# Optimization experiments

Measured on AMD Instinct MI355X. Metric: run time of the kernel, lower is better.

Reference implementation:

```python
import jax, jax.numpy as jnp
import numpy as np
import math

H = 8
D_MODEL = 512
D_K = D_MODEL // H          # 64, per-head value dim
D_QK = D_K // 2             # 32, per-head query/key dim
B, S = 2, 4096


def setup_inputs() -> dict:
    key = jax.random.key(0)
    ks = jax.random.split(key, 20)
    std = 0.02
    inp = {
        'query': jax.random.normal(ks[0], (B, S, D_MODEL), jnp.float32),
        'key':   jax.random.normal(ks[1], (B, S, D_MODEL), jnp.float32),
        'value': jax.random.normal(ks[2], (B, S, D_MODEL), jnp.float32),
        # MLP_q: d_model -> 2*d_model -> d_model/2
        'Wq1': jax.random.normal(ks[3], (D_MODEL, 2 * D_MODEL), jnp.float32) * std,
        'bq1': jnp.zeros((2 * D_MODEL,), jnp.float32),
        'Wq2': jax.random.normal(ks[4], (2 * D_MODEL, D_MODEL // 2), jnp.float32) * std,
        'bq2': jnp.zeros((D_MODEL // 2,), jnp.float32),
        # MLP_k: d_model -> 2*d_model -> d_model/2
        'Wk1': jax.random.normal(ks[5], (D_MODEL, 2 * D_MODEL), jnp.float32) * std,
        'bk1': jnp.zeros((2 * D_MODEL,), jnp.float32),
        'Wk2': jax.random.normal(ks[6], (2 * D_MODEL, D_MODEL // 2), jnp.float32) * std,
        'bk2': jnp.zeros((D_MODEL // 2,), jnp.float32),
        # linear_v and output linear: d_model -> d_model
        'Wv': jax.random.normal(ks[7], (D_MODEL, D_MODEL), jnp.float32) * std,
        'bv': jnp.zeros((D_MODEL,), jnp.float32),
        'Wo': jax.random.normal(ks[8], (D_MODEL, D_MODEL), jnp.float32) * std,
        'bo': jnp.zeros((D_MODEL,), jnp.float32),
    }
    return inp


def reference(query, key, value, Wq1, bq1, Wq2, bq2, Wk1, bk1, Wk2, bk2, Wv, bv, Wo, bo):
    nb = query.shape[0]
    # MLP_q / MLP_k: Linear -> exact GELU -> Linear (torch GELU default is erf)
    q = jax.nn.gelu(query @ Wq1 + bq1, approximate=False) @ Wq2 + bq2   # [B,S,D_MODEL/2]
    k = jax.nn.gelu(key   @ Wk1 + bk1, approximate=False) @ Wk2 + bk2   # [B,S,D_MODEL/2]
    v = value @ Wv + bv                                                  # [B,S,D_MODEL]

    q = q.reshape(nb, -1, H, D_QK)   # [B,S,H,d_qk]
    k = k.reshape(nb, -1, H, D_QK)
    v = v.reshape(nb, -1, H, D_K)    # [B,S,H,d_k]

    # scores scaled by sqrt(d_qk) since query.size(-1) == d_k//2 in the original
    scores = jnp.einsum('bqhd,bkhd->bhqk', q, k) / math.sqrt(D_QK)  # [B,H,S,S]
    p = jax.nn.softmax(scores, axis=-1)
    x = jnp.einsum('bhqk,bkhd->bqhd', p, v).reshape(nb, -1, H * D_K)  # [B,S,D_MODEL]
    return x @ Wo + bo
```

## Files before the change

### kernel.cpp

```cpp
#include <hip/hip_runtime.h>
#include <math.h>

typedef __attribute__((ext_vector_type(8))) short short8;
typedef __bf16 bf16x8 __attribute__((ext_vector_type(8)));
typedef __attribute__((ext_vector_type(4))) float f32x4;
typedef __attribute__((ext_vector_type(2))) float f32x2;
typedef __attribute__((ext_vector_type(16))) float f32x16;
typedef __attribute__((ext_vector_type(4))) unsigned uint4v;

__device__ inline short f2bf(float f) {
    unsigned u = __builtin_bit_cast(unsigned, f);
    u += 0x7fff + ((u >> 16) & 1);
    return (short)(u >> 16);
}
__device__ inline float bf2f(short h) {
    return __builtin_bit_cast(float, ((unsigned)(unsigned short)h) << 16);
}
__device__ inline float gelu_f(float x) {
    return 0.5f * x * (1.f + erff(x * 0.70710678118654752f));
}

__device__ inline void gload_lds16(const void* g, void* l) {
    __builtin_amdgcn_global_load_lds(
        (const __attribute__((address_space(1))) unsigned int*)g,
        (__attribute__((address_space(3))) unsigned int*)l, 16, 0, 0);
}

__global__ __launch_bounds__(256) void prep_all(
    const float* __restrict__ q, const float* __restrict__ k,
    const float* __restrict__ v,
    short* __restrict__ qc, short* __restrict__ kc, short* __restrict__ vc,
    const float* __restrict__ Wq1, const float* __restrict__ Wk1,
    const float* __restrict__ Wq2, const float* __restrict__ Wk2,
    const float* __restrict__ Wv,  const float* __restrict__ Wo,
    short* __restrict__ Wq1t, short* __restrict__ Wk1t,
    short* __restrict__ Wq2t, short* __restrict__ Wk2t,
    short* __restrict__ Wvt,  short* __restrict__ Wot)
{
    int id = blockIdx.x;
    if (id < 6144) {
        const float* src = id < 2048 ? q : (id < 4096 ? k : v);
        short* dst = id < 2048 ? qc : (id < 4096 ? kc : vc);
        int blk = id & 2047;
        size_t i = ((size_t)blk * 256 + threadIdx.x) * 8;
        float4 a = *(const float4*)(src + i);
        float4 b = *(const float4*)(src + i + 4);
        short8 o;
        o[0] = f2bf(a.x); o[1] = f2bf(a.y); o[2] = f2bf(a.z); o[3] = f2bf(a.w);
        o[4] = f2bf(b.x); o[5] = f2bf(b.y); o[6] = f2bf(b.z); o[7] = f2bf(b.w);
        *(short8*)(void*)(dst + i) = o;
        return;
    }
    id -= 6144;
    const float* W; short* Wt; int K, N;
    if (id < 512)       { W = Wq1; Wt = Wq1t; K = 512;  N = 1024; }
    else if (id < 1024) { W = Wk1; Wt = Wk1t; K = 512;  N = 1024; id -= 512; }
    else if (id < 1280) { W = Wq2; Wt = Wq2t; K = 1024; N = 256;  id -= 1024; }
    else if (id < 1536) { W = Wk2; Wt = Wk2t; K = 1024; N = 256;  id -= 1280; }
    else if (id < 1792) { W = Wv;  Wt = Wvt;  K = 512;  N = 512;  id -= 1536; }
    else                { W = Wo;  Wt = Wot;  K = 512;  N = 512;  id -= 1792; }
    int nx = N >> 5;
    int n0 = (id % nx) * 32, k0 = (id / nx) * 32;

    __shared__ float T[32][33];
    int tid = threadIdx.x;
    int r = tid >> 3, c4 = (tid & 7) * 4;
    float4 v4 = *(const float4*)&W[(size_t)(k0 + r) * N + n0 + c4];
    T[r][c4 + 0] = v4.x; T[r][c4 + 1] = v4.y; T[r][c4 + 2] = v4.z; T[r][c4 + 3] = v4.w;
    __syncthreads();
    short4 o;
    o.x = f2bf(T[c4 + 0][r]);
    o.y = f2bf(T[c4 + 1][r]);
    o.z = f2bf(T[c4 + 2][r]);
    o.w = f2bf(T[c4 + 3][r]);
    *(short4*)&Wt[(size_t)(n0 + r) * K + k0 + c4] = o;
}

template <int ACT, int OUTF32, int BM, int BN>
__global__ __launch_bounds__(256) void gemm_bt(
    const short* __restrict__ A0, const short* __restrict__ A1,
    const short* __restrict__ B0, const short* __restrict__ B1,
    const float* __restrict__ b0, const float* __restrict__ b1,
    void* C0_, void* C1_,
    float s0, float s1, int nbn, int N, int K)
{
    constexpr int MT = BM / 32;
    constexpr int NT = BN / 32;
    const int z = blockIdx.z;
    const short* A = z ? A1 : A0;
    const short* B = z ? B1 : B0;
    const float* bias = z ? b1 : b0;
    void* C_ = z ? C1_ : C0_;
    const float scale = z ? s1 : s0;

    const int L = blockIdx.x;
    const int xcd = L & 7;
    const int per = L >> 3;
    const int bn = (per % nbn) * BN;
    const int bm = ((per / nbn) * 8 + xcd) * BM;

    const int tid = threadIdx.x;
    const int w = tid >> 6;
    const int lane = tid & 63;
    const int l15 = lane & 15, quad = lane >> 4;
    const int wm = (w >> 1) * (BM / 2), wn = (w & 1) * (BN / 2);

    __shared__ __align__(16) short As[BM * 64];
    __shared__ __align__(16) short Bs[BN * 64];

    f32x4 acc[MT][NT];
#pragma unroll
    for (int mt = 0; mt < MT; ++mt)
#pragma unroll
        for (int nt = 0; nt < NT; ++nt) acc[mt][nt] = (f32x4){0.f, 0.f, 0.f, 0.f};

    for (int k0 = 0; k0 < K; k0 += 64) {
#pragma unroll
        for (int i = 0; i < BM / 32; ++i) {
            int ga = tid + i * 256;
            int row = ga >> 3, g = ga & 7;
            gload_lds16(&A[(size_t)(bm + row) * K + k0 + ((g ^ (row & 7)) * 8)],
                        &As[(i * 256 + w * 64) * 8]);
        }
#pragma unroll
        for (int i = 0; i < BN / 32; ++i) {
            int gb = tid + i * 256;
            int row = gb >> 3, g = gb & 7;
            gload_lds16(&B[(size_t)(bn + row) * K + k0 + ((g ^ (row & 7)) * 8)],
                        &Bs[(i * 256 + w * 64) * 8]);
        }
        __syncthreads();

#pragma unroll
        for (int ks = 0; ks < 2; ++ks) {
            bf16x8 af[MT], bfr[NT];
#pragma unroll
            for (int t = 0; t < MT; ++t) {
                int row = wm + t * 16 + l15;
                af[t] = __builtin_bit_cast(bf16x8,
                    *(const short8*)(const void*)&As[row * 64 + (((ks * 4 + quad) ^ (row & 7)) * 8)]);
            }
#pragma unroll
            for (int t = 0; t < NT; ++t) {
                int row = wn + t * 16 + l15;
                bfr[t] = __builtin_bit_cast(bf16x8,
                    *(const short8*)(const void*)&Bs[row * 64 + (((ks * 4 + quad) ^ (row & 7)) * 8)]);
            }
#pragma unroll
            for (int mt = 0; mt < MT; ++mt)
#pragma unroll
                for (int nt = 0; nt < NT; ++nt)
                    acc[mt][nt] = __builtin_amdgcn_mfma_f32_16x16x32_bf16(af[mt], bfr[nt], acc[mt][nt], 0, 0, 0);
        }
        __syncthreads();
    }

    float bv[NT];
#pragma unroll
    for (int nt = 0; nt < NT; ++nt) bv[nt] = bias[bn + wn + nt * 16 + l15];
#pragma unroll
    for (int mt = 0; mt < MT; ++mt)
#pragma unroll
        for (int r = 0; r < 4; ++r) {
            int row = bm + wm + mt * 16 + quad * 4 + r;
#pragma unroll
            for (int nt = 0; nt < NT; ++nt) {
                float v = acc[mt][nt][r] + bv[nt];
                if (ACT) v = gelu_f(v);
                v *= scale;
                int col = bn + wn + nt * 16 + l15;
                if (OUTF32) ((float*)C_)[(size_t)row * N + col] = v;
                else        ((short*)C_)[(size_t)row * N + col] = f2bf(v);
            }
        }
}

__global__ __launch_bounds__(256) void repack_kv(
    const short* __restrict__ kb, short* __restrict__ kfr,
    const short* __restrict__ vbb, short* __restrict__ vfr)
{
    const int kt = blockIdx.x;
    const int y = blockIdx.y;
    const int t = threadIdx.x;
    __shared__ short Vt[64][72];

    if (y < 16) {
        const int bh = y;
        const int b = bh >> 3, h = bh & 7;
        const int c = t >> 6, l = t & 63;
        const int nt = c >> 1, ks = c & 1;
        int key = kt * 64 + nt * 32 + (l & 31);
        int k = ks * 16 + (l >> 5) * 8;
        short8 v = *(const short8*)(const void*)&kb[(size_t)(b * 4096 + key) * 256 + h * 32 + k];
        *(short8*)(void*)&kfr[((((size_t)bh * 64 + kt) * 4 + c) * 64 + l) * 8] = v;
        return;
    }
    const int bh = y - 16;
    const int b = bh >> 3, h = bh & 7;
#pragma unroll
    for (int it = 0; it < 2; ++it) {
        int idx = t + it * 256;
        int keyr = idx >> 3, c8 = (idx & 7) * 8;
        *(short8*)(void*)&Vt[keyr][c8] =
            *(const short8*)(const void*)&vbb[(size_t)(b * 4096 + kt * 64 + keyr) * 512 + h * 64 + c8];
    }
    __syncthreads();
#pragma unroll
    for (int it = 0; it < 2; ++it) {
        int chunk = (t >> 6) * 2 + it;
        int l = t & 63;
        int dt = chunk >> 2, ks = chunk & 3;
        short8 o;
#pragma unroll
        for (int j = 0; j < 8; ++j)
            o[j] = Vt[ks * 16 + (l >> 5) * 8 + j][dt * 32 + (l & 31)];
        *(short8*)(void*)&vfr[((((size_t)bh * 64 + kt) * 8 + chunk) * 64 + l) * 8] = o;
    }
}

__global__ __launch_bounds__(256, 4) void flash_ks(
    const short* __restrict__ qb, const short* __restrict__ kfr,
    const short* __restrict__ vfr, short* __restrict__ xbb)
{
    const int L = blockIdx.x;
    const int xcd = L & 7;
    const int idx = L >> 3;
    const int bh = xcd * 2 + (idx & 1);
    const int qt = idx >> 1;
    const int b = bh >> 3, h = bh & 7;
    const int w = threadIdx.x >> 6;
    const int qg = w >> 1;
    const int kh = w & 1;
    const int lane = threadIdx.x & 63;
    const int l31 = lane & 31;
    const int half = lane >> 5;

    __shared__ __align__(16) char smem[17408];

    const short* qrow = qb + (size_t)(b * 4096 + qt * 64 + qg * 32 + l31) * 256 + h * 32 + half * 8;
    bf16x8 qf0 = __builtin_bit_cast(bf16x8, *(const short8*)(const void*)qrow);
    bf16x8 qf1 = __builtin_bit_cast(bf16x8, *(const short8*)(const void*)(qrow + 16));

    f32x16 O0{}, O1{};
    f32x2 lp = (f32x2){0.f, 0.f};

    const short* kbase = kfr + ((size_t)bh * 64) * 4 * 512 + lane * 8;
    const short* vbase = vfr + ((size_t)bh * 64) * 8 * 512 + lane * 8;

#pragma unroll 1
    for (int t = 0; t < 32; ++t) {
        const int kt = kh * 32 + t;
        bf16x8 kc[4], vc[8];
        const short* kp = kbase + (size_t)kt * 4 * 512;
        const short* vp = vbase + (size_t)kt * 8 * 512;
#pragma unroll
        for (int c = 0; c < 4; ++c)
            kc[c] = __builtin_bit_cast(bf16x8, *(const short8*)(const void*)(kp + c * 512));
#pragma unroll
        for (int c = 0; c < 8; ++c)
            vc[c] = __builtin_bit_cast(bf16x8, *(const short8*)(const void*)(vp + c * 512));

        f32x16 zero{};
        f32x16 s0 = __builtin_amdgcn_mfma_f32_32x32x16_bf16(kc[0], qf0, zero, 0, 0, 0);
        s0 = __builtin_amdgcn_mfma_f32_32x32x16_bf16(kc[1], qf1, s0, 0, 0, 0);
        f32x16 s1 = __builtin_amdgcn_mfma_f32_32x32x16_bf16(kc[2], qf0, zero, 0, 0, 0);
        s1 = __builtin_amdgcn_mfma_f32_32x32x16_bf16(kc[3], qf1, s1, 0, 0, 0);

        bf16x8 pf[4];
#pragma unroll
        for (int nt = 0; nt < 2; ++nt) {
            const f32x16& s = nt ? s1 : s0;
            float p0  = __builtin_amdgcn_exp2f(s[0]);
            float p1  = __builtin_amdgcn_exp2f(s[1]);
            float p2  = __builtin_amdgcn_exp2f(s[2]);
            float p3  = __builtin_amdgcn_exp2f(s[3]);
            float p4  = __builtin_amdgcn_exp2f(s[4]);
            float p5  = __builtin_amdgcn_exp2f(s[5]);
            float p6  = __builtin_amdgcn_exp2f(s[6]);
            float p7  = __builtin_amdgcn_exp2f(s[7]);
            float p8  = __builtin_amdgcn_exp2f(s[8]);
            float p9  = __builtin_amdgcn_exp2f(s[9]);
            float p10 = __builtin_amdgcn_exp2f(s[10]);
            float p11 = __builtin_amdgcn_exp2f(s[11]);
            float p12 = __builtin_amdgcn_exp2f(s[12]);
            float p13 = __builtin_amdgcn_exp2f(s[13]);
            float p14 = __builtin_amdgcn_exp2f(s[14]);
            float p15 = __builtin_amdgcn_exp2f(s[15]);

            lp += (f32x2){p0,  p1};
            lp += (f32x2){p2,  p3};
            lp += (f32x2){p4,  p5};
            lp += (f32x2){p6,  p7};
            lp += (f32x2){p8,  p9};
            lp += (f32x2){p10, p11};
            lp += (f32x2){p12, p13};
            lp += (f32x2){p14, p15};

            unsigned D0, D1, D2, D3, D4, D5, D6, D7;
            asm("v_cvt_pk_bf16_f32 %0, %1, %2" : "=v"(D0) : "v"(p0),  "v"(p1));
            asm("v_cvt_pk_bf16_f32 %0, %1, %2" : "=v"(D1) : "v"(p2),  "v"(p3));
            asm("v_cvt_pk_bf16_f32 %0, %1, %2" : "=v"(D2) : "v"(p4),  "v"(p5));
            asm("v_cvt_pk_bf16_f32 %0, %1, %2" : "=v"(D3) : "v"(p6),  "v"(p7));
            asm("v_cvt_pk_bf16_f32 %0, %1, %2" : "=v"(D4) : "v"(p8),  "v"(p9));
            asm("v_cvt_pk_bf16_f32 %0, %1, %2" : "=v"(D5) : "v"(p10), "v"(p11));
            asm("v_cvt_pk_bf16_f32 %0, %1, %2" : "=v"(D6) : "v"(p12), "v"(p13));
            asm("v_cvt_pk_bf16_f32 %0, %1, %2" : "=v"(D7) : "v"(p14), "v"(p15));
            asm("v_permlane32_swap_b32 %0, %1" : "+v"(D0), "+v"(D2));
            asm("v_permlane32_swap_b32 %0, %1" : "+v"(D1), "+v"(D3));
            asm("v_permlane32_swap_b32 %0, %1" : "+v"(D4), "+v"(D6));
            asm("v_permlane32_swap_b32 %0, %1" : "+v"(D5), "+v"(D7));
            uint4v u0; u0[0] = D0; u0[1] = D1; u0[2] = D2; u0[3] = D3;
            uint4v u1; u1[0] = D4; u1[1] = D5; u1[2] = D6; u1[3] = D7;
            pf[2 * nt + 0] = __builtin_bit_cast(bf16x8, u0);
            pf[2 * nt + 1] = __builtin_bit_cast(bf16x8, u1);
        }

#pragma unroll
        for (int ks = 0; ks < 4; ++ks) {
            O0 = __builtin_amdgcn_mfma_f32_32x32x16_bf16(pf[ks], vc[ks], O0, 0, 0, 0);
            O1 = __builtin_amdgcn_mfma_f32_32x32x16_bf16(pf[ks], vc[4 + ks], O1, 0, 0, 0);
        }
    }

    float lsum = lp[0] + lp[1];
    float lother = lsum;
    asm("v_permlane32_swap_b32 %0, %1" : "+v"(lsum), "+v"(lother));
    lsum += lother;

    float* redO = (float*)smem;
    float* redl = (float*)(smem + 16896);
    if (half == 0)
        redl[(qg * 2 + kh) * 32 + l31] = lsum;
    if (kh == 1) {
        float* Bo = redO + qg * 32 * 66;
#pragma unroll
        for (int r = 0; r < 16; ++r) {
            int q = (r & 3) + 8 * (r >> 2) + 4 * half;
            Bo[q * 66 + l31] = O0[r];
            Bo[q * 66 + 32 + l31] = O1[r];
        }
    }
    __syncthreads();
    if (kh == 0) {
        const float* Bo = redO + qg * 32 * 66;
#pragma unroll
        for (int r = 0; r < 16; ++r) {
            int q = (r & 3) + 8 * (r >> 2) + 4 * half;
            float o0 = O0[r] + Bo[q * 66 + l31];
            float o1 = O1[r] + Bo[q * 66 + 32 + l31];
            float inv = 1.f / (redl[(qg * 2 + 0) * 32 + q] + redl[(qg * 2 + 1) * 32 + q]);
            size_t row = (size_t)(b * 4096 + qt * 64 + qg * 32 + q);
            short* d = xbb + row * 512 + h * 64 + l31;
            d[0] = f2bf(o0 * inv);
            d[32] = f2bf(o1 * inv);
        }
    }
}

extern "C" void kernel_launch(void* const* d_in, const int* in_sizes, int n_in,
                              void* d_out, int out_size, void* d_ws, size_t ws_size,
                              hipStream_t stream)
{
    const float* query = (const float*)d_in[0];
    const float* key   = (const float*)d_in[1];
    const float* value = (const float*)d_in[2];
    const float* Wq1   = (const float*)d_in[3];
    const float* bq1   = (const float*)d_in[4];
    const float* Wq2   = (const float*)d_in[5];
    const float* bq2   = (const float*)d_in[6];
    const float* Wk1   = (const float*)d_in[7];
    const float* bk1   = (const float*)d_in[8];
    const float* Wk2   = (const float*)d_in[9];
    const float* bk2   = (const float*)d_in[10];
    const float* Wv    = (const float*)d_in[11];
    const float* bv    = (const float*)d_in[12];
    const float* Wo    = (const float*)d_in[13];
    const float* bo    = (const float*)d_in[14];
    float* out = (float*)d_out;

    char* ws = (char*)d_ws;
    short* H1q   = (short*)(ws + 0);
    short* H1k   = (short*)(ws + 16777216);
    short* xbb   = (short*)(ws + 0);
    short* qcast = (short*)(ws + 33554432);
    short* kcast = (short*)(ws + 41943040);
    short* vcast = (short*)(ws + 50331648);
    short* qbb   = (short*)(ws + 33554432);
    short* kbb   = (short*)(ws + 37748736);
    short* vbb   = (short*)(ws + 41943040);
    short* kfr   = (short*)(ws + 50331648);
    short* vfr   = (short*)(ws + 54525952);
    short* Wq1t  = (short*)(ws + 62914560);
    short* Wk1t  = (short*)(ws + 63963136);
    short* Wq2t  = (short*)(ws + 65011712);
    short* Wk2t  = (short*)(ws + 65536000);
    short* Wvt   = (short*)(ws + 66060288);
    short* Wot   = (short*)(ws + 66584576);

    dim3 blk(256);
    const float qscale = 0.17677669529663687f * 1.4426950408889634f;

    prep_all<<<dim3(8192), blk, 0, stream>>>(
        query, key, value, qcast, kcast, vcast,
        Wq1, Wk1, Wq2, Wk2, Wv, Wo, Wq1t, Wk1t, Wq2t, Wk2t, Wvt, Wot);

    gemm_bt<1, 0, 128, 128><<<dim3(8 * 64, 1, 2), blk, 0, stream>>>(
        qcast, kcast, Wq1t, Wk1t, bq1, bk1, H1q, H1k, 1.f, 1.f, 8, 1024, 512);
    gemm_bt<0, 0, 64, 64><<<dim3(4 * 128, 1, 2), blk, 0, stream>>>(
        H1q, H1k, Wq2t, Wk2t, bq2, bk2, qbb, kbb, qscale, 1.f, 4, 256, 1024);
    gemm_bt<0, 0, 64, 64><<<dim3(8 * 128, 1, 1), blk, 0, stream>>>(
        vcast, vcast, Wvt, Wvt, bv, bv, vbb, vbb, 1.f, 1.f, 8, 512, 512);
    repack_kv<<<dim3(64, 32), blk, 0, stream>>>(kbb, kfr, vbb, vfr);
    flash_ks<<<dim3(1024), blk, 0, stream>>>(qbb, kfr, vfr, xbb);
    gemm_bt<0, 1, 64, 64><<<dim3(8 * 128, 1, 1), blk, 0, stream>>>(
        xbb, xbb, Wot, Wot, bo, bo, out, out, 1.f, 1.f, 8, 512, 512);
}
```

Before: 260.0 us.

## Fuse input fp32-to-bf16 casts into GEMMs and write K/V in fragment layout

Removes the separate cast pass over query/key/value by having the first-layer GEMMs load fp32 A tiles directly and convert them to bf16 in registers before storing to LDS. Also drops the repack_kv kernel: the K-projection and V-projection GEMM epilogues scatter outputs straight into the MFMA fragment layouts that the flash kernel consumes. This saves two kernel launches and a full read/write round trip of the activations. In exchange, the fp32 A path uses synchronous register loads instead of async global-to-LDS loads and moves twice the bytes per tile, and the scattered epilogue stores are poorly coalesced.

```diff
diff --git a/kernel.cpp b/kernel.cpp
--- a/kernel.cpp
+++ b/kernel.cpp
@@ -13,9 +13,6 @@
     u += 0x7fff + ((u >> 16) & 1);
     return (short)(u >> 16);
 }
-__device__ inline float bf2f(short h) {
-    return __builtin_bit_cast(float, ((unsigned)(unsigned short)h) << 16);
-}
 __device__ inline float gelu_f(float x) {
     return 0.5f * x * (1.f + erff(x * 0.70710678118654752f));
 }
@@ -26,10 +23,7 @@
         (__attribute__((address_space(3))) unsigned int*)l, 16, 0, 0);
 }
 
-__global__ __launch_bounds__(256) void prep_all(
-    const float* __restrict__ q, const float* __restrict__ k,
-    const float* __restrict__ v,
-    short* __restrict__ qc, short* __restrict__ kc, short* __restrict__ vc,
+__global__ __launch_bounds__(256) void prep_w(
     const float* __restrict__ Wq1, const float* __restrict__ Wk1,
     const float* __restrict__ Wq2, const float* __restrict__ Wk2,
     const float* __restrict__ Wv,  const float* __restrict__ Wo,
@@ -38,20 +32,6 @@
     short* __restrict__ Wvt,  short* __restrict__ Wot)
 {
     int id = blockIdx.x;
-    if (id < 6144) {
-        const float* src = id < 2048 ? q : (id < 4096 ? k : v);
-        short* dst = id < 2048 ? qc : (id < 4096 ? kc : vc);
-        int blk = id & 2047;
-        size_t i = ((size_t)blk * 256 + threadIdx.x) * 8;
-        float4 a = *(const float4*)(src + i);
-        float4 b = *(const float4*)(src + i + 4);
-        short8 o;
-        o[0] = f2bf(a.x); o[1] = f2bf(a.y); o[2] = f2bf(a.z); o[3] = f2bf(a.w);
-        o[4] = f2bf(b.x); o[5] = f2bf(b.y); o[6] = f2bf(b.z); o[7] = f2bf(b.w);
-        *(short8*)(void*)(dst + i) = o;
-        return;
-    }
-    id -= 6144;
     const float* W; short* Wt; int K, N;
     if (id < 512)       { W = Wq1; Wt = Wq1t; K = 512;  N = 1024; }
     else if (id < 1024) { W = Wk1; Wt = Wk1t; K = 512;  N = 1024; id -= 512; }
@@ -76,9 +56,9 @@
     *(short4*)&Wt[(size_t)(n0 + r) * K + k0 + c4] = o;
 }
 
-template <int ACT, int OUTF32, int BM, int BN>
+template <int ACT, int AF32, int OM0, int OM1, int BM, int BN>
 __global__ __launch_bounds__(256) void gemm_bt(
-    const short* __restrict__ A0, const short* __restrict__ A1,
+    const void* __restrict__ A0, const void* __restrict__ A1,
     const short* __restrict__ B0, const short* __restrict__ B1,
     const float* __restrict__ b0, const float* __restrict__ b1,
     void* C0_, void* C1_,
@@ -87,11 +67,12 @@
     constexpr int MT = BM / 32;
     constexpr int NT = BN / 32;
     const int z = blockIdx.z;
-    const short* A = z ? A1 : A0;
+    const void* A = z ? A1 : A0;
     const short* B = z ? B1 : B0;
     const float* bias = z ? b1 : b0;
     void* C_ = z ? C1_ : C0_;
     const float scale = z ? s1 : s0;
+    const int om = z ? OM1 : OM0;
 
     const int L = blockIdx.x;
     const int xcd = L & 7;
@@ -119,8 +100,23 @@
         for (int i = 0; i < BM / 32; ++i) {
             int ga = tid + i * 256;
             int row = ga >> 3, g = ga & 7;
-            gload_lds16(&A[(size_t)(bm + row) * K + k0 + ((g ^ (row & 7)) * 8)],
-                        &As[(i * 256 + w * 64) * 8]);
+            if constexpr (AF32) {
+                const float* Af = (const float*)A;
+                const float* src = &Af[(size_t)(bm + row) * K + k0 + ((g ^ (row & 7)) * 8)];
+                float4 x = *(const float4*)src;
+                float4 y = *(const float4*)(src + 4);
+                unsigned u0, u1, u2, u3;
+                asm("v_cvt_pk_bf16_f32 %0, %1, %2" : "=v"(u0) : "v"(x.x), "v"(x.y));
+                asm("v_cvt_pk_bf16_f32 %0, %1, %2" : "=v"(u1) : "v"(x.z), "v"(x.w));
+                asm("v_cvt_pk_bf16_f32 %0, %1, %2" : "=v"(u2) : "v"(y.x), "v"(y.y));
+                asm("v_cvt_pk_bf16_f32 %0, %1, %2" : "=v"(u3) : "v"(y.z), "v"(y.w));
+                uint4v u; u[0] = u0; u[1] = u1; u[2] = u2; u[3] = u3;
+                *(uint4v*)(void*)&As[row * 64 + g * 8] = u;
+            } else {
+                const short* Ab = (const short*)A;
+                gload_lds16(&Ab[(size_t)(bm + row) * K + k0 + ((g ^ (row & 7)) * 8)],
+                            &As[(i * 256 + w * 64) * 8]);
+            }
         }
 #pragma unroll
         for (int i = 0; i < BN / 32; ++i) {
@@ -155,9 +151,9 @@
         __syncthreads();
     }
 
-    float bv[NT];
-#pragma unroll
-    for (int nt = 0; nt < NT; ++nt) bv[nt] = bias[bn + wn + nt * 16 + l15];
+    float bvv[NT];
+#pragma unroll
+    for (int nt = 0; nt < NT; ++nt) bvv[nt] = bias[bn + wn + nt * 16 + l15];
 #pragma unroll
     for (int mt = 0; mt < MT; ++mt)
 #pragma unroll
@@ -165,57 +161,34 @@
             int row = bm + wm + mt * 16 + quad * 4 + r;
 #pragma unroll
             for (int nt = 0; nt < NT; ++nt) {
-                float v = acc[mt][nt][r] + bv[nt];
+                float v = acc[mt][nt][r] + bvv[nt];
                 if (ACT) v = gelu_f(v);
                 v *= scale;
                 int col = bn + wn + nt * 16 + l15;
-                if (OUTF32) ((float*)C_)[(size_t)row * N + col] = v;
-                else        ((short*)C_)[(size_t)row * N + col] = f2bf(v);
+                if (om == 1) {
+                    ((float*)C_)[(size_t)row * N + col] = v;
+                } else if (om == 2) {
+                    int b_ = row >> 12, key = row & 4095;
+                    int kt = key >> 6, nt_ = (key >> 5) & 1, l31_ = key & 31;
+                    int h_ = col >> 5, kcol = col & 31;
+                    int ks_ = kcol >> 4, hi_ = (kcol >> 3) & 1, j_ = kcol & 7;
+                    size_t idx = ((((size_t)(b_ * 8 + h_) * 64 + kt) * 4 +
+                                   (nt_ * 2 + ks_)) * 64 + (hi_ * 32 + l31_)) * 8 + j_;
+                    ((short*)C_)[idx] = f2bf(v);
+                } else if (om == 3) {
+                    int b_ = row >> 12, key = row & 4095;
+                    int kt = key >> 6, keyr = key & 63;
+                    int ks_ = keyr >> 4, hi_ = (keyr >> 3) & 1, j_ = keyr & 7;
+                    int h_ = col >> 6, dk = col & 63;
+                    int dt_ = dk >> 5, l31_ = dk & 31;
+                    size_t idx = ((((size_t)(b_ * 8 + h_) * 64 + kt) * 8 +
+                                   (dt_ * 4 + ks_)) * 64 + (hi_ * 32 + l31_)) * 8 + j_;
+                    ((short*)C_)[idx] = f2bf(v);
+                } else {
+                    ((short*)C_)[(size_t)row * N + col] = f2bf(v);
+                }
             }
         }
-}
-
-__global__ __launch_bounds__(256) void repack_kv(
-    const short* __restrict__ kb, short* __restrict__ kfr,
-    const short* __restrict__ vbb, short* __restrict__ vfr)
-{
-    const int kt = blockIdx.x;
-    const int y = blockIdx.y;
-    const int t = threadIdx.x;
-    __shared__ short Vt[64][72];
-
-    if (y < 16) {
-        const int bh = y;
-        const int b = bh >> 3, h = bh & 7;
-        const int c = t >> 6, l = t & 63;
-        const int nt = c >> 1, ks = c & 1;
-        int key = kt * 64 + nt * 32 + (l & 31);
-        int k = ks * 16 + (l >> 5) * 8;
-        short8 v = *(const short8*)(const void*)&kb[(size_t)(b * 4096 + key) * 256 + h * 32 + k];
-        *(short8*)(void*)&kfr[((((size_t)bh * 64 + kt) * 4 + c) * 64 + l) * 8] = v;
-        return;
-    }
-    const int bh = y - 16;
-    const int b = bh >> 3, h = bh & 7;
-#pragma unroll
-    for (int it = 0; it < 2; ++it) {
-        int idx = t + it * 256;
-        int keyr = idx >> 3, c8 = (idx & 7) * 8;
-        *(short8*)(void*)&Vt[keyr][c8] =
-            *(const short8*)(const void*)&vbb[(size_t)(b * 4096 + kt * 64 + keyr) * 512 + h * 64 + c8];
-    }
-    __syncthreads();
-#pragma unroll
-    for (int it = 0; it < 2; ++it) {
-        int chunk = (t >> 6) * 2 + it;
-        int l = t & 63;
-        int dt = chunk >> 2, ks = chunk & 3;
-        short8 o;
-#pragma unroll
-        for (int j = 0; j < 8; ++j)
-            o[j] = Vt[ks * 16 + (l >> 5) * 8 + j][dt * 32 + (l & 31)];
-        *(short8*)(void*)&vfr[((((size_t)bh * 64 + kt) * 8 + chunk) * 64 + l) * 8] = o;
-    }
 }
 
 __global__ __launch_bounds__(256, 4) void flash_ks(
@@ -382,12 +355,7 @@
     short* H1q   = (short*)(ws + 0);
     short* H1k   = (short*)(ws + 16777216);
     short* xbb   = (short*)(ws + 0);
-    short* qcast = (short*)(ws + 33554432);
-    short* kcast = (short*)(ws + 41943040);
-    short* vcast = (short*)(ws + 50331648);
     short* qbb   = (short*)(ws + 33554432);
-    short* kbb   = (short*)(ws + 37748736);
-    short* vbb   = (short*)(ws + 41943040);
     short* kfr   = (short*)(ws + 50331648);
     short* vfr   = (short*)(ws + 54525952);
     short* Wq1t  = (short*)(ws + 62914560);
@@ -400,18 +368,16 @@
     dim3 blk(256);
     const float qscale = 0.17677669529663687f * 1.4426950408889634f;
 
-    prep_all<<<dim3(8192), blk, 0, stream>>>(
-        query, key, value, qcast, kcast, vcast,
+    prep_w<<<dim3(2048), blk, 0, stream>>>(
         Wq1, Wk1, Wq2, Wk2, Wv, Wo, Wq1t, Wk1t, Wq2t, Wk2t, Wvt, Wot);
 
-    gemm_bt<1, 0, 128, 128><<<dim3(8 * 64, 1, 2), blk, 0, stream>>>(
-        qcast, kcast, Wq1t, Wk1t, bq1, bk1, H1q, H1k, 1.f, 1.f, 8, 1024, 512);
-    gemm_bt<0, 0, 64, 64><<<dim3(4 * 128, 1, 2), blk, 0, stream>>>(
-        H1q, H1k, Wq2t, Wk2t, bq2, bk2, qbb, kbb, qscale, 1.f, 4, 256, 1024);
-    gemm_bt<0, 0, 64, 64><<<dim3(8 * 128, 1, 1), blk, 0, stream>>>(
-        vcast, vcast, Wvt, Wvt, bv, bv, vbb, vbb, 1.f, 1.f, 8, 512, 512);
-    repack_kv<<<dim3(64, 32), blk, 0, stream>>>(kbb, kfr, vbb, vfr);
+    gemm_bt<1, 1, 0, 0, 128, 128><<<dim3(8 * 64, 1, 2), blk, 0, stream>>>(
+        query, key, Wq1t, Wk1t, bq1, bk1, H1q, H1k, 1.f, 1.f, 8, 1024, 512);
+    gemm_bt<0, 0, 0, 2, 64, 64><<<dim3(4 * 128, 1, 2), blk, 0, stream>>>(
+        H1q, H1k, Wq2t, Wk2t, bq2, bk2, qbb, kfr, qscale, 1.f, 4, 256, 1024);
+    gemm_bt<0, 1, 3, 3, 64, 64><<<dim3(8 * 128, 1, 1), blk, 0, stream>>>(
+        value, value, Wvt, Wvt, bv, bv, vfr, vfr, 1.f, 1.f, 8, 512, 512);
     flash_ks<<<dim3(1024), blk, 0, stream>>>(qbb, kfr, vfr, xbb);
-    gemm_bt<0, 1, 64, 64><<<dim3(8 * 128, 1, 1), blk, 0, stream>>>(
+    gemm_bt<0, 0, 1, 1, 64, 64><<<dim3(8 * 128, 1, 1), blk, 0, stream>>>(
         xbb, xbb, Wot, Wot, bo, bo, out, out, 1.f, 1.f, 8, 512, 512);
 }
```

After: 259.4 us. About the same (-0.2%).
